# Performance work log

Hardware: AMD Instinct MI355X
Metric: run time of the kernel (lower is better)

Reference implementation:

```python
import jax, jax.numpy as jnp
import numpy as np
from jax import lax

DH = 256   # d_hidden
NL = 8     # number of wavenet cells
K = 3      # kernel_size
DIN = 16   # d_lag + d_cov
DOUT = 1
T, B = 1024, 64


def setup_inputs() -> dict:
    key = jax.random.key(0)
    ks = jax.random.split(key, 20)
    s = 0.05
    inp = {
        "X_emb": jax.random.randint(ks[0], (T, B, 1), 0, 10),
        "X_cov": jax.random.normal(ks[1], (T, B, 8), jnp.float32),
        "X_lag": jax.random.normal(ks[2], (T, B, 8), jnp.float32),
        "y": jax.random.normal(ks[3], (T, B, DOUT), jnp.float32),
        "domain": jax.random.uniform(ks[4], (B, 4), jnp.float32),
        "up_w": jax.random.normal(ks[5], (DIN, DH), jnp.float32) * s,
        "up_b": jnp.zeros((DH,), jnp.float32),
        "conv_dil_w": jax.random.normal(ks[6], (NL, 2 * DH, DH, K), jnp.float32) * s,
        "conv_dil_b": jnp.zeros((NL, 2 * DH), jnp.float32),
        "skip_w": jax.random.normal(ks[7], (NL, 2 * DH, DH), jnp.float32) * s,
        "skip_b": jnp.zeros((NL, 2 * DH), jnp.float32),
        "fc_w": jax.random.normal(ks[8], (DH, DH), jnp.float32) * s,
        "fc_b": jnp.zeros((DH,), jnp.float32),
        "loc_w": jax.random.normal(ks[9], (DH, DOUT), jnp.float32) * s,
        "loc_b": jnp.zeros((DOUT,), jnp.float32),
        "scale_w": jax.random.normal(ks[10], (DH, DOUT), jnp.float32) * s,
        "scale_b": jnp.zeros((DOUT,), jnp.float32),
        "d_outputseqlen": 24,
    }
    return inp


def _causal_conv(h, w, b, dil):
    # h: [B, C, T], w: [O, C, K] -> causal (left-padded) dilated conv
    pad = (w.shape[-1] - 1) * dil
    y = lax.conv_general_dilated(h, w, window_strides=(1,), padding=[(pad, 0)],
                                 rhs_dilation=(dil,),
                                 dimension_numbers=("NCH", "OIH", "NCH"))
    return y + b[None, :, None]


def _forward(X_cov, X_lag, y, up_w, up_b, conv_dil_w, conv_dil_b,
             skip_w, skip_b, fc_w, fc_b, loc_w, loc_b, scale_w, scale_b,
             d_outputseqlen):
    t = X_lag.shape[0]
    h = jnp.concatenate([X_lag, X_cov[:t]], axis=-1) @ up_w + up_b  # [T,B,DH]
    h = jnp.transpose(h, (1, 2, 0))  # [B, DH, T]
    skip = jnp.zeros_like(h)
    for i in range(NL):
        fg = _causal_conv(h, conv_dil_w[i], conv_dil_b[i], 2 ** i)  # [B,2DH,T]
        f, g = jnp.split(fg, 2, axis=1)
        gated = jnp.tanh(f) * jax.nn.sigmoid(g)  # [B,DH,T]
        hs = jnp.einsum("oc,bct->bot", skip_w[i], gated) + skip_b[i][None, :, None]
        h_next, skip_next = jnp.split(hs, 2, axis=1)
        h = h + h_next
        skip = skip + skip_next
    feat = jnp.transpose(skip, (2, 0, 1))  # [T,B,DH]
    ff = jax.nn.relu(feat @ fc_w + fc_b)
    tail = ff[-d_outputseqlen:]
    loc = tail @ loc_w + loc_b
    scale = jax.nn.softplus(tail @ scale_w + scale_b) + 1e-6
    yt = y[-d_outputseqlen:]
    log_prob = (-0.5 * ((yt - loc) / scale) ** 2
                - jnp.log(scale) - 0.5 * np.log(2.0 * np.pi))
    loss_y = -jnp.mean(log_prob)
    total_loss = loss_y  # loss_d forced to 0 in the original forward
    return total_loss, loss_y, loc, scale


def reference(X_emb, X_cov, X_lag, y, domain, up_w, up_b, conv_dil_w,
              conv_dil_b, skip_w, skip_b, fc_w, fc_b, loc_w, loc_b,
              scale_w, scale_b, d_outputseqlen):
    # X_emb and domain are unused with d_emb=[] and loss_d hard-set to 0.
    return _forward(X_cov, X_lag, y, up_w, up_b, conv_dil_w, conv_dil_b,
                    skip_w, skip_b, fc_w, fc_b, loc_w, loc_b,
                    scale_w, scale_b, d_outputseqlen)
```

## Files before the change

kernel.cpp:

```cpp
#include <hip/hip_runtime.h>
#include <math.h>

static constexpr int TT = 1024, BB = 64, DHID = 256, NLAY = 8, OSL = 24;

typedef __attribute__((ext_vector_type(8))) short short8;
typedef __attribute__((ext_vector_type(4))) float f32x4;
typedef unsigned short u16;
typedef __attribute__((ext_vector_type(4))) unsigned short u16x4;
typedef unsigned int u32;

__device__ __forceinline__ u16 f2bf(float x) {
  u32 u = __float_as_uint(x);
  return (u16)((u + 0x7fffu + ((u >> 16) & 1u)) >> 16);
}

__device__ __forceinline__ void gll16(const u16* g, u16* l) {
  __builtin_amdgcn_global_load_lds((const __attribute__((address_space(1))) void*)g,
                                   (__attribute__((address_space(3))) void*)l, 16, 0, 0);
}

__global__ __launch_bounds__(256) void wprep(
    const float* __restrict__ cw, const float* __restrict__ sw,
    u16* __restrict__ wT, u16* __restrict__ swT)
{
  const int stride = gridDim.x * 256;
  for (int idx = blockIdx.x * 256 + threadIdx.x; idx < NLAY * 3 * 512 * 256; idx += stride) {
    const int c = idx & 255;
    const int o = (idx >> 8) & 511;
    const int lt = idx >> 17;
    const int tap = lt % 3, l = lt / 3;
    wT[idx] = f2bf(cw[((size_t)(l * 512 + o) * 256 + c) * 3 + tap]);
  }
  for (int idx = blockIdx.x * 256 + threadIdx.x; idx < NLAY * 512 * 256; idx += stride)
    swT[idx] = f2bf(sw[idx]);
}

__global__ __launch_bounds__(256) void up_kernel(
    const float* __restrict__ xlag, const float* __restrict__ xcov,
    const float* __restrict__ upw, const float* __restrict__ upb,
    float* __restrict__ h, u16* __restrict__ hb0)
{
  const int b  = blockIdx.y;
  const int t0 = blockIdx.x * 16;
  __shared__ float xs[16][17];
  {
    const int tl = threadIdx.x >> 4;
    const int j  = threadIdx.x & 15;
    const size_t base = ((size_t)(t0 + tl) * BB + b) * 8;
    xs[tl][j] = (j < 8) ? xlag[base + j] : xcov[base + (j - 8)];
  }
  __syncthreads();
  const int c = threadIdx.x;
  float uw[16];
#pragma unroll
  for (int j = 0; j < 16; ++j) uw[j] = upw[j * DHID + c];
  const float bias = upb[c];
#pragma unroll
  for (int tl = 0; tl < 16; ++tl) {
    float acc = bias;
#pragma unroll
    for (int j = 0; j < 16; ++j) acc = fmaf(xs[tl][j], uw[j], acc);
    const size_t idx = ((size_t)b * TT + t0 + tl) * DHID + c;
    h[idx]   = acc;
    hb0[idx] = f2bf(acc);
  }
}

__global__ __launch_bounds__(512, 4) void layer_fused(
    const u16* __restrict__ hbin, const u16* __restrict__ wT,
    const float* __restrict__ cb, const u16* __restrict__ swT,
    const float* __restrict__ sb, float* __restrict__ hf,
    u16* __restrict__ hbout, float* __restrict__ skipf,
    const int dil, const int tile0)
{
  __shared__ u16 As[512 * 32];
  __shared__ u16 Bs[64 * 32];
  __shared__ u16 gLDS[64 * 264];

  const int b    = blockIdx.y;
  const int tile = tile0 + blockIdx.x;
  const int t0   = tile * 64;
  const bool last = (tile == 15);
  const int tid = threadIdx.x, w = tid >> 6, lane = tid & 63;
  const int l16 = lane & 15, quad = lane >> 4;
  const u16* hb = hbin + (size_t)b * TT * DHID;

  f32x4 acc[4][4];
  const f32x4 zero = {0.f, 0.f, 0.f, 0.f};
#pragma unroll
  for (int m = 0; m < 4; ++m)
#pragma unroll
    for (int n = 0; n < 4; ++n) acc[m][n] = zero;

  for (int tap = 0; tap < 3; ++tap) {
    const int sh = (2 - tap) * dil;
    const u16* wtap = wT + (size_t)tap * 512 * 256;
    for (int kc = 0; kc < 8; ++kc) {
      const int c0 = kc * 32;
#pragma unroll
      for (int q = 0; q < 4; ++q) {
        const int lin = q * 512 + tid;
        gll16(wtap + (size_t)(lin >> 2) * 256 + c0 + (lin & 3) * 8,
              As + (size_t)(q * 512 + (tid & ~63)) * 8);
      }
      if (w < 4) {
        const int tl = 16 * w + (lane >> 2);
        gll16(hb + (size_t)(t0 - sh + tl) * 256 + c0 + (lane & 3) * 8,
              Bs + w * 512);
      }
      __syncthreads();
      short8 bfr[4], afr[4];
#pragma unroll
      for (int nt = 0; nt < 4; ++nt)
        bfr[nt] = *(const short8*)&Bs[(nt * 16 + l16) * 32 + quad * 8];
#pragma unroll
      for (int m = 0; m < 4; ++m) {
        const int o = ((m & 2) ? 256 : 0) + 32 * w + (m & 1) * 16 + l16;
        afr[m] = *(const short8*)&As[(size_t)o * 32 + quad * 8];
      }
#pragma unroll
      for (int m = 0; m < 4; ++m)
#pragma unroll
        for (int nt = 0; nt < 4; ++nt)
          acc[m][nt] = __builtin_amdgcn_mfma_f32_16x16x32_bf16(afr[m], bfr[nt], acc[m][nt], 0, 0, 0);
      __syncthreads();
    }
  }

#pragma unroll
  for (int mf = 0; mf < 2; ++mf) {
#pragma unroll
    for (int nt = 0; nt < 4; ++nt) {
      u16x4 pk;
#pragma unroll
      for (int r = 0; r < 4; ++r) {
        const int c = 32 * w + mf * 16 + quad * 4 + r;
        const float f = acc[mf][nt][r] + cb[c];
        const float g = acc[mf + 2][nt][r] + cb[256 + c];
        const float th = 2.f / (1.f + __expf(-2.f * f)) - 1.f;
        const float sg = 1.f / (1.f + __expf(-g));
        pk[r] = f2bf(th * sg);
      }
      *(u16x4*)&gLDS[(size_t)(nt * 16 + l16) * 264 + 32 * w + mf * 16 + quad * 4] = pk;
    }
  }
  __syncthreads();

#pragma unroll
  for (int m = 0; m < 4; ++m)
#pragma unroll
    for (int n = 0; n < 4; ++n) acc[m][n] = zero;

  const int nq = last ? 4 : 2;
  for (int kc = 0; kc < 8; ++kc) {
    const int c0 = kc * 32;
    for (int q = 0; q < nq; ++q) {
      const int lin = q * 512 + tid;
      gll16(swT + (size_t)(lin >> 2) * 256 + c0 + (lin & 3) * 8,
            As + (size_t)(q * 512 + (tid & ~63)) * 8);
    }
    __syncthreads();
    short8 bfr[4];
#pragma unroll
    for (int nt = 0; nt < 4; ++nt)
      bfr[nt] = *(const short8*)&gLDS[(size_t)(nt * 16 + l16) * 264 + c0 + quad * 8];
#pragma unroll
    for (int m = 0; m < 2; ++m) {
      const int o = 32 * w + m * 16 + l16;
      short8 a = *(const short8*)&As[(size_t)o * 32 + quad * 8];
#pragma unroll
      for (int nt = 0; nt < 4; ++nt)
        acc[m][nt] = __builtin_amdgcn_mfma_f32_16x16x32_bf16(a, bfr[nt], acc[m][nt], 0, 0, 0);
    }
    if (last) {
#pragma unroll
      for (int m = 2; m < 4; ++m) {
        const int o = 256 + 32 * w + (m & 1) * 16 + l16;
        short8 a = *(const short8*)&As[(size_t)o * 32 + quad * 8];
#pragma unroll
        for (int nt = 0; nt < 4; ++nt)
          acc[m][nt] = __builtin_amdgcn_mfma_f32_16x16x32_bf16(a, bfr[nt], acc[m][nt], 0, 0, 0);
      }
    }
    __syncthreads();
  }

#pragma unroll
  for (int mh = 0; mh < 2; ++mh) {
#pragma unroll
    for (int nt = 0; nt < 4; ++nt) {
      const int t  = t0 + nt * 16 + l16;
      const int c4 = 32 * w + mh * 16 + quad * 4;
      const size_t idx = ((size_t)b * TT + t) * DHID + c4;
      f32x4 hv = *(f32x4*)&hf[idx];
      u16x4 pk;
#pragma unroll
      for (int r = 0; r < 4; ++r) {
        const float v = hv[r] + acc[mh][nt][r] + sb[c4 + r];
        hv[r] = v;
        pk[r] = f2bf(v);
      }
      *(f32x4*)&hf[idx] = hv;
      *(u16x4*)&hbout[idx] = pk;
    }
  }
  if (last) {
#pragma unroll
    for (int mh = 0; mh < 2; ++mh) {
#pragma unroll
      for (int nt = 0; nt < 4; ++nt) {
        const int tl = nt * 16 + l16;
        const int c4 = 32 * w + mh * 16 + quad * 4;
        const size_t idx = ((size_t)b * 64 + tl) * DHID + c4;
        f32x4 sv = *(f32x4*)&skipf[idx];
#pragma unroll
        for (int r = 0; r < 4; ++r)
          sv[r] += acc[mh + 2][nt][r] + sb[256 + c4 + r];
        *(f32x4*)&skipf[idx] = sv;
      }
    }
  }
}

__global__ __launch_bounds__(256) void head_kernel(
    const float* __restrict__ skipf,
    const float* __restrict__ fcw, const float* __restrict__ fcb,
    const float* __restrict__ locw, const float* __restrict__ locb,
    const float* __restrict__ scw, const float* __restrict__ scb,
    float* __restrict__ out)
{
  const int tt = blockIdx.x;
  const int b  = blockIdx.y;
  const int tl = 40 + tt;
  const int c  = threadIdx.x;
  __shared__ float xs[DHID];
  xs[c] = skipf[((size_t)b * 64 + tl) * DHID + c];
  __syncthreads();
  float acc = fcb[c];
#pragma unroll 8
  for (int j = 0; j < DHID; ++j) acc = fmaf(xs[j], fcw[j * DHID + c], acc);
  const float ff = fmaxf(acc, 0.f);
  float pl = ff * locw[c];
  float ps = ff * scw[c];
#pragma unroll
  for (int off = 32; off > 0; off >>= 1) {
    pl += __shfl_down(pl, off);
    ps += __shfl_down(ps, off);
  }
  __shared__ float rl[4], rs[4];
  const int wid = threadIdx.x >> 6, lane = threadIdx.x & 63;
  if (lane == 0) { rl[wid] = pl; rs[wid] = ps; }
  __syncthreads();
  if (threadIdx.x == 0) {
    const float loc = rl[0] + rl[1] + rl[2] + rl[3] + locb[0];
    const float x   = rs[0] + rs[1] + rs[2] + rs[3] + scb[0];
    const float sp  = (x > 0.f) ? (x + log1pf(expf(-x))) : log1pf(expf(x));
    out[2 + tt * BB + b]            = loc;
    out[2 + OSL * BB + tt * BB + b] = sp + 1e-6f;
  }
}

__global__ __launch_bounds__(256) void loss_kernel(
    const float* __restrict__ y, float* __restrict__ out)
{
  float s = 0.f;
  for (int i = threadIdx.x; i < OSL * BB; i += 256) {
    const int tt = i >> 6, b = i & 63;
    const float loc = out[2 + i];
    const float sc  = out[2 + OSL * BB + i];
    const float yt  = y[(size_t)(TT - OSL + tt) * BB + b];
    const float z   = (yt - loc) / sc;
    s += -0.5f * z * z - logf(sc) - 0.9189385332046727f;
  }
#pragma unroll
  for (int off = 32; off > 0; off >>= 1) s += __shfl_down(s, off);
  __shared__ float r[4];
  if ((threadIdx.x & 63) == 0) r[threadIdx.x >> 6] = s;
  __syncthreads();
  if (threadIdx.x == 0) {
    const float loss = -(r[0] + r[1] + r[2] + r[3]) / (float)(OSL * BB);
    out[0] = loss;
    out[1] = loss;
  }
}

extern "C" void kernel_launch(void* const* d_in, const int* in_sizes, int n_in,
                              void* d_out, int out_size, void* d_ws, size_t ws_size,
                              hipStream_t stream) {
  (void)in_sizes; (void)n_in; (void)out_size; (void)ws_size;
  const float* X_cov  = (const float*)d_in[1];
  const float* X_lag  = (const float*)d_in[2];
  const float* y      = (const float*)d_in[3];
  const float* up_w   = (const float*)d_in[5];
  const float* up_b   = (const float*)d_in[6];
  const float* conv_w = (const float*)d_in[7];
  const float* conv_b = (const float*)d_in[8];
  const float* skip_w = (const float*)d_in[9];
  const float* skip_b = (const float*)d_in[10];
  const float* fc_w   = (const float*)d_in[11];
  const float* fc_b   = (const float*)d_in[12];
  const float* loc_w  = (const float*)d_in[13];
  const float* loc_b  = (const float*)d_in[14];
  const float* sc_w   = (const float*)d_in[15];
  const float* sc_b   = (const float*)d_in[16];

  float* hf    = (float*)d_ws;
  u16*   hb0   = (u16*)  ((char*)d_ws + 67108864);
  u16*   hb1   = (u16*)  ((char*)d_ws + 100663296);
  float* skipf = (float*)((char*)d_ws + 134217728);
  u16*   wT    = (u16*)  ((char*)d_ws + 138412032);
  u16*   swT   = (u16*)  ((char*)d_ws + 144703488);

  wprep<<<2048, 256, 0, stream>>>(conv_w, skip_w, wT, swT);
  hipMemsetAsync(skipf, 0, (size_t)BB * 64 * DHID * sizeof(float), stream);
  up_kernel<<<dim3(TT / 16, BB), 256, 0, stream>>>(X_lag, X_cov, up_w, up_b, hf, hb0);

  static const int Ptab[NLAY] = {4, 5, 6, 7, 8, 9, 11, 15};
  u16* hin = hb0;
  u16* hout = hb1;
  for (int i = 0; i < NLAY; ++i) {
    const int ntiles = 16 - Ptab[i];
    layer_fused<<<dim3(ntiles, BB), 512, 0, stream>>>(
        hin, wT + (size_t)i * 3 * 512 * 256, conv_b + i * 512,
        swT + (size_t)i * 512 * 256, skip_b + i * 512,
        hf, hout, skipf, 1 << i, Ptab[i]);
    u16* tmp = hin; hin = hout; hout = tmp;
  }

  head_kernel<<<dim3(OSL, BB), 256, 0, stream>>>(
      skipf, fc_w, fc_b, loc_w, loc_b, sc_w, sc_b, (float*)d_out);
  loss_kernel<<<1, 256, 0, stream>>>(y, (float*)d_out);
}
```

Baseline: 734.3 us.

## Split layer into conv-gate and skip kernels with batched tiles and packed layouts

```diff
diff --git a/kernel.cpp b/kernel.cpp
--- a/kernel.cpp
+++ b/kernel.cpp
@@ -2,6 +2,8 @@
 #include <math.h>
 
 static constexpr int TT = 1024, BB = 64, DHID = 256, NLAY = 8, OSL = 24;
+static constexpr int T0H = 192, THN = 832;
+static constexpr int T0G = 256, TGN = 768;
 
 typedef __attribute__((ext_vector_type(8))) short short8;
 typedef __attribute__((ext_vector_type(4))) float f32x4;
@@ -13,7 +15,9 @@
   u32 u = __float_as_uint(x);
   return (u16)((u + 0x7fffu + ((u >> 16) & 1u)) >> 16);
 }
-
+__device__ __forceinline__ float bf2f(u16 v) {
+  return __uint_as_float((u32)v << 16);
+}
 __device__ __forceinline__ void gll16(const u16* g, u16* l) {
   __builtin_amdgcn_global_load_lds((const __attribute__((address_space(1))) void*)g,
                                    (__attribute__((address_space(3))) void*)l, 16, 0, 0);
@@ -21,27 +25,35 @@
 
 __global__ __launch_bounds__(256) void wprep(
     const float* __restrict__ cw, const float* __restrict__ sw,
-    u16* __restrict__ wT, u16* __restrict__ swT)
+    u16* __restrict__ wP, u16* __restrict__ swH, u16* __restrict__ swG)
 {
   const int stride = gridDim.x * 256;
-  for (int idx = blockIdx.x * 256 + threadIdx.x; idx < NLAY * 3 * 512 * 256; idx += stride) {
-    const int c = idx & 255;
-    const int o = (idx >> 8) & 511;
-    const int lt = idx >> 17;
-    const int tap = lt % 3, l = lt / 3;
-    wT[idx] = f2bf(cw[((size_t)(l * 512 + o) * 256 + c) * 3 + tap]);
-  }
-  for (int idx = blockIdx.x * 256 + threadIdx.x; idx < NLAY * 512 * 256; idx += stride)
-    swT[idx] = f2bf(sw[idx]);
+  for (int i = blockIdx.x * 256 + threadIdx.x; i < NLAY * 3 * 8 * 2 * 4 * 2048; i += stride) {
+    const int e = i & 7, row = (i >> 3) & 255;
+    int q = i >> 11;
+    const int p = q & 3; q >>= 2;
+    const int cs = q & 1; q >>= 1;
+    const int kc = q & 7; q >>= 3;
+    const int tap = q % 3, l = q / 3;
+    const int o = (row < 128) ? (cs * 128 + row) : (256 + cs * 128 + (row - 128));
+    const int c = kc * 32 + p * 8 + e;
+    wP[i] = f2bf(cw[((size_t)(l * 512 + o) * 256 + c) * 3 + tap]);
+  }
+  for (int i = blockIdx.x * 256 + threadIdx.x; i < NLAY * 8 * 4 * 2048; i += stride) {
+    const int e = i & 7, o = (i >> 3) & 255, p = (i >> 11) & 3, kc = (i >> 13) & 7, l = i >> 16;
+    const int c = kc * 32 + p * 8 + e;
+    swH[i] = f2bf(sw[(size_t)(l * 512 + o) * 256 + c]);
+    swG[i] = f2bf(sw[(size_t)(l * 512 + 256 + o) * 256 + c]);
+  }
 }
 
 __global__ __launch_bounds__(256) void up_kernel(
     const float* __restrict__ xlag, const float* __restrict__ xcov,
     const float* __restrict__ upw, const float* __restrict__ upb,
-    float* __restrict__ h, u16* __restrict__ hb0)
+    u16* __restrict__ hb0)
 {
   const int b  = blockIdx.y;
-  const int t0 = blockIdx.x * 16;
+  const int t0 = T0H + blockIdx.x * 16;
   __shared__ float xs[16][17];
   {
     const int tl = threadIdx.x >> 4;
@@ -60,170 +72,227 @@
     float acc = bias;
 #pragma unroll
     for (int j = 0; j < 16; ++j) acc = fmaf(xs[tl][j], uw[j], acc);
-    const size_t idx = ((size_t)b * TT + t0 + tl) * DHID + c;
-    h[idx]   = acc;
-    hb0[idx] = f2bf(acc);
-  }
-}
-
-__global__ __launch_bounds__(512, 4) void layer_fused(
-    const u16* __restrict__ hbin, const u16* __restrict__ wT,
-    const float* __restrict__ cb, const u16* __restrict__ swT,
-    const float* __restrict__ sb, float* __restrict__ hf,
-    u16* __restrict__ hbout, float* __restrict__ skipf,
-    const int dil, const int tile0)
-{
-  __shared__ u16 As[512 * 32];
-  __shared__ u16 Bs[64 * 32];
-  __shared__ u16 gLDS[64 * 264];
-
-  const int b    = blockIdx.y;
-  const int tile = tile0 + blockIdx.x;
-  const int t0   = tile * 64;
-  const bool last = (tile == 15);
+    hb0[(((size_t)b * 32 + (c >> 3)) * THN + (t0 + tl - T0H)) * 8 + (c & 7)] = f2bf(acc);
+  }
+}
+
+__global__ __launch_bounds__(1024) void conv_gate(
+    const u16* __restrict__ hbin, const u16* __restrict__ wPl,
+    const float* __restrict__ cb, u16* __restrict__ gbuf,
+    u16* __restrict__ g15l, const int dil, const int tile0)
+{
+  __shared__ u16 AB[2][16384];
   const int tid = threadIdx.x, w = tid >> 6, lane = tid & 63;
   const int l16 = lane & 15, quad = lane >> 4;
-  const u16* hb = hbin + (size_t)b * TT * DHID;
+  const int mw = w & 3, nw = w >> 2;
+  const int tile = tile0 + (int)(blockIdx.x >> 4);
+  const int b0 = (blockIdx.x & 15) * 4;
+  const int cs = blockIdx.y;
+  const int t0 = tile * 64;
 
   f32x4 acc[4][4];
   const f32x4 zero = {0.f, 0.f, 0.f, 0.f};
 #pragma unroll
   for (int m = 0; m < 4; ++m)
 #pragma unroll
-    for (int n = 0; n < 4; ++n) acc[m][n] = zero;
-
-  for (int tap = 0; tap < 3; ++tap) {
+    for (int j = 0; j < 4; ++j) acc[m][j] = zero;
+
+  const int ctb = tid >> 8, pb = (tid >> 6) & 3, tlb = tid & 63;
+
+  auto stage = [&](int buf, int tap, int kc) {
+    gll16(wPl + (size_t)(((tap * 8 + kc) * 2 + cs)) * 8192 + tid * 8,
+          &AB[buf][(tid & ~63) * 8]);
     const int sh = (2 - tap) * dil;
-    const u16* wtap = wT + (size_t)tap * 512 * 256;
-    for (int kc = 0; kc < 8; ++kc) {
-      const int c0 = kc * 32;
-#pragma unroll
-      for (int q = 0; q < 4; ++q) {
-        const int lin = q * 512 + tid;
-        gll16(wtap + (size_t)(lin >> 2) * 256 + c0 + (lin & 3) * 8,
-              As + (size_t)(q * 512 + (tid & ~63)) * 8);
-      }
-      if (w < 4) {
-        const int tl = 16 * w + (lane >> 2);
-        gll16(hb + (size_t)(t0 - sh + tl) * 256 + c0 + (lane & 3) * 8,
-              Bs + w * 512);
-      }
-      __syncthreads();
-      short8 bfr[4], afr[4];
-#pragma unroll
-      for (int nt = 0; nt < 4; ++nt)
-        bfr[nt] = *(const short8*)&Bs[(nt * 16 + l16) * 32 + quad * 8];
-#pragma unroll
-      for (int m = 0; m < 4; ++m) {
-        const int o = ((m & 2) ? 256 : 0) + 32 * w + (m & 1) * 16 + l16;
-        afr[m] = *(const short8*)&As[(size_t)o * 32 + quad * 8];
-      }
-#pragma unroll
-      for (int m = 0; m < 4; ++m)
-#pragma unroll
-        for (int nt = 0; nt < 4; ++nt)
-          acc[m][nt] = __builtin_amdgcn_mfma_f32_16x16x32_bf16(afr[m], bfr[nt], acc[m][nt], 0, 0, 0);
-      __syncthreads();
-    }
-  }
-
-#pragma unroll
-  for (int mf = 0; mf < 2; ++mf) {
-#pragma unroll
-    for (int nt = 0; nt < 4; ++nt) {
+    gll16(hbin + (((size_t)(b0 + ctb) * 32 + kc * 4 + pb) * THN + (t0 - sh - T0H + tlb)) * 8,
+          &AB[buf][8192 + (tid & ~63) * 8]);
+  };
+
+  stage(0, 0, 0);
+  __syncthreads();
+  for (int step = 0; step < 24; ++step) {
+    const int ns = step + 1;
+    if (ns < 24) stage(ns & 1, ns >> 3, ns & 7);
+    const u16* A = AB[step & 1];
+    const u16* B = AB[step & 1] + 8192;
+    short8 bfr[4];
+#pragma unroll
+    for (int j = 0; j < 4; ++j)
+      bfr[j] = *(const short8*)&B[(nw * 256 + quad * 64 + 16 * j + l16) * 8];
+#pragma unroll
+    for (int m = 0; m < 4; ++m) {
+      const int rowbase = (m < 2) ? (mw * 32 + 16 * m) : (128 + mw * 32 + 16 * (m - 2));
+      const short8 a = *(const short8*)&A[(quad * 256 + rowbase + l16) * 8];
+#pragma unroll
+      for (int j = 0; j < 4; ++j)
+        acc[m][j] = __builtin_amdgcn_mfma_f32_16x16x32_bf16(a, bfr[j], acc[m][j], 0, 0, 0);
+    }
+    __syncthreads();
+  }
+
+  u16* gT = (u16*)AB;
+#pragma unroll
+  for (int m = 0; m < 2; ++m) {
+    const int c4 = mw * 32 + 16 * m + quad * 4;
+    const int cpl = c4 >> 3;
+#pragma unroll
+    for (int j = 0; j < 4; ++j) {
+      const int tl = 16 * j + l16;
       u16x4 pk;
 #pragma unroll
       for (int r = 0; r < 4; ++r) {
-        const int c = 32 * w + mf * 16 + quad * 4 + r;
-        const float f = acc[mf][nt][r] + cb[c];
-        const float g = acc[mf + 2][nt][r] + cb[256 + c];
+        const float f = acc[m][j][r]     + cb[cs * 128 + c4 + r];
+        const float g = acc[m + 2][j][r] + cb[256 + cs * 128 + c4 + r];
         const float th = 2.f / (1.f + __expf(-2.f * f)) - 1.f;
         const float sg = 1.f / (1.f + __expf(-g));
         pk[r] = f2bf(th * sg);
       }
-      *(u16x4*)&gLDS[(size_t)(nt * 16 + l16) * 264 + 32 * w + mf * 16 + quad * 4] = pk;
-    }
-  }
-  __syncthreads();
-
+      *(u16x4*)&gT[((nw * 16 + cpl) * 64 + tl) * 8 + (quad & 1) * 4] = pk;
+    }
+  }
+  __syncthreads();
+#pragma unroll
+  for (int k = 0; k < 4; ++k) {
+    const int slot = k * 1024 + tid;
+    const int ct = slot >> 10, cpl = (slot >> 6) & 15, tl = slot & 63;
+    const short8 v = *(const short8*)&gT[slot * 8];
+    const int b = b0 + ct, cpg = cs * 16 + cpl;
+    *(short8*)&gbuf[(((size_t)b * 32 + cpg) * TGN + (t0 + tl - T0G)) * 8] = v;
+    if (tile == 15)
+      *(short8*)&g15l[(((size_t)b * 32 + cpg) * 64 + tl) * 8] = v;
+  }
+}
+
+__global__ __launch_bounds__(1024) void skip_h(
+    const u16* __restrict__ gbuf, const u16* __restrict__ swHl,
+    const float* __restrict__ sb, const u16* __restrict__ hbin,
+    u16* __restrict__ hbout, const int tile0)
+{
+  __shared__ u16 AB[2][16384];
+  const int tid = threadIdx.x, w = tid >> 6, lane = tid & 63;
+  const int l16 = lane & 15, quad = lane >> 4;
+  const int mw = w & 3, nw = w >> 2;
+  const int tile = tile0 + (int)(blockIdx.x >> 4);
+  const int b0 = (blockIdx.x & 15) * 4;
+  const int t0 = tile * 64;
+
+  f32x4 acc[4][4];
+  const f32x4 zero = {0.f, 0.f, 0.f, 0.f};
 #pragma unroll
   for (int m = 0; m < 4; ++m)
 #pragma unroll
-    for (int n = 0; n < 4; ++n) acc[m][n] = zero;
-
-  const int nq = last ? 4 : 2;
-  for (int kc = 0; kc < 8; ++kc) {
-    const int c0 = kc * 32;
-    for (int q = 0; q < nq; ++q) {
-      const int lin = q * 512 + tid;
-      gll16(swT + (size_t)(lin >> 2) * 256 + c0 + (lin & 3) * 8,
-            As + (size_t)(q * 512 + (tid & ~63)) * 8);
+    for (int j = 0; j < 4; ++j) acc[m][j] = zero;
+
+  const int ctb = tid >> 8, pb = (tid >> 6) & 3, tlb = tid & 63;
+
+  auto stage = [&](int buf, int kc) {
+    gll16(swHl + (size_t)kc * 8192 + tid * 8, &AB[buf][(tid & ~63) * 8]);
+    gll16(gbuf + (((size_t)(b0 + ctb) * 32 + kc * 4 + pb) * TGN + (t0 - T0G + tlb)) * 8,
+          &AB[buf][8192 + (tid & ~63) * 8]);
+  };
+
+  stage(0, 0);
+  __syncthreads();
+  for (int step = 0; step < 8; ++step) {
+    if (step + 1 < 8) stage((step + 1) & 1, step + 1);
+    const u16* A = AB[step & 1];
+    const u16* B = AB[step & 1] + 8192;
+    short8 bfr[4];
+#pragma unroll
+    for (int j = 0; j < 4; ++j)
+      bfr[j] = *(const short8*)&B[(nw * 256 + quad * 64 + 16 * j + l16) * 8];
+#pragma unroll
+    for (int m = 0; m < 4; ++m) {
+      const short8 a = *(const short8*)&A[(quad * 256 + mw * 64 + 16 * m + l16) * 8];
+#pragma unroll
+      for (int j = 0; j < 4; ++j)
+        acc[m][j] = __builtin_amdgcn_mfma_f32_16x16x32_bf16(a, bfr[j], acc[m][j], 0, 0, 0);
     }
     __syncthreads();
-    short8 bfr[4];
-#pragma unroll
-    for (int nt = 0; nt < 4; ++nt)
-      bfr[nt] = *(const short8*)&gLDS[(size_t)(nt * 16 + l16) * 264 + c0 + quad * 8];
-#pragma unroll
-    for (int m = 0; m < 2; ++m) {
-      const int o = 32 * w + m * 16 + l16;
-      short8 a = *(const short8*)&As[(size_t)o * 32 + quad * 8];
-#pragma unroll
-      for (int nt = 0; nt < 4; ++nt)
-        acc[m][nt] = __builtin_amdgcn_mfma_f32_16x16x32_bf16(a, bfr[nt], acc[m][nt], 0, 0, 0);
-    }
-    if (last) {
-#pragma unroll
-      for (int m = 2; m < 4; ++m) {
-        const int o = 256 + 32 * w + (m & 1) * 16 + l16;
-        short8 a = *(const short8*)&As[(size_t)o * 32 + quad * 8];
-#pragma unroll
-        for (int nt = 0; nt < 4; ++nt)
-          acc[m][nt] = __builtin_amdgcn_mfma_f32_16x16x32_bf16(a, bfr[nt], acc[m][nt], 0, 0, 0);
+  }
+
+  float* fT = (float*)AB;
+  for (int ctr = 0; ctr < 4; ++ctr) {
+    __syncthreads();
+    if (nw == ctr) {
+#pragma unroll
+      for (int m = 0; m < 4; ++m) {
+        const int c4 = mw * 64 + 16 * m + quad * 4;
+#pragma unroll
+        for (int j = 0; j < 4; ++j) {
+          const int tl = 16 * j + l16;
+          f32x4 v;
+#pragma unroll
+          for (int r = 0; r < 4; ++r) v[r] = acc[m][j][r] + sb[c4 + r];
+          *(f32x4*)&fT[((c4 >> 3) * 64 + tl) * 8 + (quad & 1) * 4] = v;
+        }
       }
     }
     __syncthreads();
-  }
-
-#pragma unroll
-  for (int mh = 0; mh < 2; ++mh) {
-#pragma unroll
-    for (int nt = 0; nt < 4; ++nt) {
-      const int t  = t0 + nt * 16 + l16;
-      const int c4 = 32 * w + mh * 16 + quad * 4;
-      const size_t idx = ((size_t)b * TT + t) * DHID + c4;
-      f32x4 hv = *(f32x4*)&hf[idx];
-      u16x4 pk;
-#pragma unroll
-      for (int r = 0; r < 4; ++r) {
-        const float v = hv[r] + acc[mh][nt][r] + sb[c4 + r];
-        hv[r] = v;
-        pk[r] = f2bf(v);
-      }
-      *(f32x4*)&hf[idx] = hv;
-      *(u16x4*)&hbout[idx] = pk;
-    }
-  }
-  if (last) {
-#pragma unroll
-    for (int mh = 0; mh < 2; ++mh) {
-#pragma unroll
-      for (int nt = 0; nt < 4; ++nt) {
-        const int tl = nt * 16 + l16;
-        const int c4 = 32 * w + mh * 16 + quad * 4;
-        const size_t idx = ((size_t)b * 64 + tl) * DHID + c4;
-        f32x4 sv = *(f32x4*)&skipf[idx];
-#pragma unroll
-        for (int r = 0; r < 4; ++r)
-          sv[r] += acc[mh + 2][nt][r] + sb[256 + c4 + r];
-        *(f32x4*)&skipf[idx] = sv;
-      }
-    }
-  }
+    const int b = b0 + ctr;
+#pragma unroll
+    for (int k = 0; k < 2; ++k) {
+      const int slot = k * 1024 + tid;
+      const int cpl = slot >> 6, tl = slot & 63;
+      const size_t idx = (((size_t)b * 32 + cpl) * THN + (t0 - T0H + tl)) * 8;
+      const short8 hv = *(const short8*)&hbin[idx];
+      short8 ov;
+#pragma unroll
+      for (int e = 0; e < 8; ++e)
+        ov[e] = (short)f2bf(bf2f((u16)hv[e]) + fT[slot * 8 + e]);
+      *(short8*)&hbout[idx] = ov;
+    }
+  }
+}
+
+__global__ __launch_bounds__(1024) void skip_g_final(
+    const u16* __restrict__ g15, const u16* __restrict__ swG,
+    float* __restrict__ skipf)
+{
+  __shared__ u16 AB[2][10240];
+  const int tid = threadIdx.x, w = tid >> 6, lane = tid & 63;
+  const int l16 = lane & 15, quad = lane >> 4;
+  const int b = blockIdx.x;
+
+  f32x4 acc[4];
+  const f32x4 zero = {0.f, 0.f, 0.f, 0.f};
+#pragma unroll
+  for (int j = 0; j < 4; ++j) acc[j] = zero;
+
+  auto stage = [&](int buf, int ks) {
+    gll16(swG + (size_t)ks * 8192 + tid * 8, &AB[buf][(tid & ~63) * 8]);
+    if (tid < 256) {
+      const int p = tid >> 6, tl = tid & 63;
+      const int l = ks >> 3, kc = ks & 7;
+      gll16(g15 + ((((size_t)l * 64 + b) * 32 + kc * 4 + p) * 64 + tl) * 8,
+            &AB[buf][8192 + (tid & ~63) * 8]);
+    }
+  };
+
+  stage(0, 0);
+  __syncthreads();
+  for (int step = 0; step < 64; ++step) {
+    if (step + 1 < 64) stage((step + 1) & 1, step + 1);
+    const u16* A = AB[step & 1];
+    const u16* B = AB[step & 1] + 8192;
+    const short8 a = *(const short8*)&A[(quad * 256 + w * 16 + l16) * 8];
+#pragma unroll
+    for (int j = 0; j < 4; ++j) {
+      const short8 bf = *(const short8*)&B[(quad * 64 + 16 * j + l16) * 8];
+      acc[j] = __builtin_amdgcn_mfma_f32_16x16x32_bf16(a, bf, acc[j], 0, 0, 0);
+    }
+    __syncthreads();
+  }
+#pragma unroll
+  for (int j = 0; j < 4; ++j)
+#pragma unroll
+    for (int r = 0; r < 4; ++r) {
+      const int c = w * 16 + quad * 4 + r;
+      skipf[((size_t)b * 256 + c) * 64 + 16 * j + l16] = acc[j][r];
+    }
 }
 
 __global__ __launch_bounds__(256) void head_kernel(
-    const float* __restrict__ skipf,
+    const float* __restrict__ skipf, const float* __restrict__ skip_b,
     const float* __restrict__ fcw, const float* __restrict__ fcb,
     const float* __restrict__ locw, const float* __restrict__ locb,
     const float* __restrict__ scw, const float* __restrict__ scb,
@@ -234,7 +303,10 @@
   const int tl = 40 + tt;
   const int c  = threadIdx.x;
   __shared__ float xs[DHID];
-  xs[c] = skipf[((size_t)b * 64 + tl) * DHID + c];
+  float sbg = 0.f;
+#pragma unroll
+  for (int l = 0; l < NLAY; ++l) sbg += skip_b[l * 512 + 256 + c];
+  xs[c] = skipf[((size_t)b * 256 + c) * 64 + tl] + sbg;
   __syncthreads();
   float acc = fcb[c];
 #pragma unroll 8
@@ -304,30 +376,34 @@
   const float* sc_w   = (const float*)d_in[15];
   const float* sc_b   = (const float*)d_in[16];
 
-  float* hf    = (float*)d_ws;
-  u16*   hb0   = (u16*)  ((char*)d_ws + 67108864);
-  u16*   hb1   = (u16*)  ((char*)d_ws + 100663296);
-  float* skipf = (float*)((char*)d_ws + 134217728);
-  u16*   wT    = (u16*)  ((char*)d_ws + 138412032);
-  u16*   swT   = (u16*)  ((char*)d_ws + 144703488);
-
-  wprep<<<2048, 256, 0, stream>>>(conv_w, skip_w, wT, swT);
-  hipMemsetAsync(skipf, 0, (size_t)BB * 64 * DHID * sizeof(float), stream);
-  up_kernel<<<dim3(TT / 16, BB), 256, 0, stream>>>(X_lag, X_cov, up_w, up_b, hf, hb0);
+  char* wsb = (char*)d_ws;
+  u16*   hb0   = (u16*)(wsb + 0);
+  u16*   hb1   = (u16*)(wsb + 27262976);
+  u16*   gbuf  = (u16*)(wsb + 54525952);
+  u16*   g15   = (u16*)(wsb + 79691776);
+  u16*   wP    = (u16*)(wsb + 96468992);
+  u16*   swH   = (u16*)(wsb + 102760448);
+  u16*   swG   = (u16*)(wsb + 103809024);
+  float* skipf = (float*)(wsb + 104857600);
+
+  wprep<<<1024, 256, 0, stream>>>(conv_w, skip_w, wP, swH, swG);
+  up_kernel<<<dim3(52, BB), 256, 0, stream>>>(X_lag, X_cov, up_w, up_b, hb0);
 
   static const int Ptab[NLAY] = {4, 5, 6, 7, 8, 9, 11, 15};
   u16* hin = hb0;
   u16* hout = hb1;
   for (int i = 0; i < NLAY; ++i) {
     const int ntiles = 16 - Ptab[i];
-    layer_fused<<<dim3(ntiles, BB), 512, 0, stream>>>(
-        hin, wT + (size_t)i * 3 * 512 * 256, conv_b + i * 512,
-        swT + (size_t)i * 512 * 256, skip_b + i * 512,
-        hf, hout, skipf, 1 << i, Ptab[i]);
+    conv_gate<<<dim3(ntiles * 16, 2), 1024, 0, stream>>>(
+        hin, wP + (size_t)i * 393216, conv_b + i * 512, gbuf,
+        g15 + (size_t)i * 1048576, 1 << i, Ptab[i]);
+    skip_h<<<dim3(ntiles * 16), 1024, 0, stream>>>(
+        gbuf, swH + (size_t)i * 65536, skip_b + i * 512, hin, hout, Ptab[i]);
     u16* tmp = hin; hin = hout; hout = tmp;
   }
 
+  skip_g_final<<<dim3(64), 1024, 0, stream>>>(g15, swG, skipf);
   head_kernel<<<dim3(OSL, BB), 256, 0, stream>>>(
-      skipf, fc_w, fc_b, loc_w, loc_b, sc_w, sc_b, (float*)d_out);
+      skipf, skip_b, fc_w, fc_b, loc_w, loc_b, sc_w, sc_b, (float*)d_out);
   loss_kernel<<<1, 256, 0, stream>>>(y, (float*)d_out);
 }
```

Result: faster. 665.8 us (-9.3%).
